# Kernel optimization log

Hardware: AMD Instinct MI355X
Metric: run time of the kernel (lower is better)

## Reference

```python
import jax, jax.numpy as jnp
import numpy as np

F_DIM = 256; H = 4; LAT = 256; BOT = 128
B = 64; NPG = 180; N = B * NPG; E = N * 16; HF = H * F_DIM
NEG_SLOPE = 0.2  # PyG GATConv default LeakyReLU slope


def _gat(x, src, dst, W, att_s, att_d, bias):
    # PyG GATConv (concat=True): h = x W, per-edge score LeakyReLU(a_s[src]+a_d[dst]),
    # softmax over incoming edges of each dst, weighted sum, concat heads, + bias.
    h = (x @ W).reshape(N, H, F_DIM)
    a_s = jnp.einsum('nhc,hc->nh', h, att_s)
    a_d = jnp.einsum('nhc,hc->nh', h, att_d)
    e = jax.nn.leaky_relu(a_s[src] + a_d[dst], NEG_SLOPE)          # [E+N, H]
    m = jax.ops.segment_max(e, dst, num_segments=N)                # stable softmax per dst
    p = jnp.exp(e - m[dst])
    s = jax.ops.segment_sum(p, dst, num_segments=N)
    alpha = p / (s[dst] + 1e-16)
    out = jax.ops.segment_sum(alpha[:, :, None] * h[src], dst, num_segments=N)
    return out.reshape(N, HF) + bias


def setup_inputs() -> dict:
    key = jax.random.key(0)
    ks = jax.random.split(key, 40)
    def rn(i, shape, scale):
        return jax.random.normal(ks[i], shape, jnp.float32) * jnp.float32(scale)
    inp = {}
    inp['z'] = jax.random.normal(ks[0], (B, LAT), jnp.float32)
    inp['condition'] = jax.random.normal(ks[1], (B, BOT), jnp.float32)
    dst = jax.random.randint(ks[2], (E,), 0, N)
    off = jax.random.randint(ks[3], (E,), 1, NPG)
    src = (dst + off) % N  # no self-loops by construction (PyG adds them itself)
    inp['edge_index'] = jnp.stack([src, dst]).astype(jnp.int32)
    inp['batch'] = jnp.repeat(jnp.arange(B, dtype=jnp.int32), NPG)
    def lin(i, fin, fout):
        s = 1.0 / np.sqrt(fin)
        return rn(i, (fin, fout), s), rn(i + 1, (fout,), s)
    inp['W_init'], inp['b_init'] = lin(4, LAT + BOT, F_DIM)
    inp['W1'] = rn(6, (F_DIM + 180, HF), 1.0 / np.sqrt(F_DIM + 180))
    inp['as1'] = rn(7, (H, F_DIM), 0.1); inp['ad1'] = rn(8, (H, F_DIM), 0.1)
    inp['b1'] = rn(9, (HF,), 0.1)
    inp['W2'] = rn(10, (HF, HF), 1.0 / np.sqrt(HF))
    inp['as2'] = rn(11, (H, F_DIM), 0.1); inp['ad2'] = rn(12, (H, F_DIM), 0.1)
    inp['b2'] = rn(13, (HF,), 0.1)
    inp['W3'] = rn(14, (HF, HF), 1.0 / np.sqrt(HF))
    inp['as3'] = rn(15, (H, F_DIM), 0.1); inp['ad3'] = rn(16, (H, F_DIM), 0.1)
    inp['b3'] = rn(17, (HF,), 0.1)
    inp['Wp'], inp['bp'] = lin(18, HF, F_DIM)
    inp['Wfp'], inp['bfp'] = lin(20, F_DIM, 2)
    inp['Ws'], inp['bs'] = lin(22, HF, F_DIM)
    inp['Wfs'], inp['bfs'] = lin(24, F_DIM, 2)
    inp['Wt'], inp['bt'] = lin(26, HF, F_DIM)
    inp['Wft'], inp['bft'] = lin(28, F_DIM, 1)
    return inp


def reference(z, condition, edge_index, batch, W_init, b_init,
              W1, as1, ad1, b1, W2, as2, ad2, b2, W3, as3, ad3, b3,
              Wp, bp, Wfp, bfp, Ws, bs, Wfs, bfs, Wt, bt, Wft, bft):
    zc = jnp.concatenate([z, condition], axis=1) @ W_init + b_init  # [B, F]
    x = zc[batch]                                                    # [N, F]
    # node order within each (sorted) batch segment -> one-hot(180)
    start = jnp.searchsorted(batch, jnp.arange(B, dtype=batch.dtype))
    order = jnp.arange(N) - start[batch]
    pos = jax.nn.one_hot(order, 180, dtype=x.dtype)
    x = jax.nn.relu(jnp.concatenate([x, pos], axis=1))               # [N, F+180]
    # add self loops (PyG GATConv default add_self_loops=True)
    loops = jnp.arange(N, dtype=edge_index.dtype)
    src = jnp.concatenate([edge_index[0], loops])
    dst = jnp.concatenate([edge_index[1], loops])
    x = jax.nn.relu(_gat(x, src, dst, W1, as1, ad1, b1))
    x = jax.nn.relu(_gat(x, src, dst, W2, as2, ad2, b2))
    x = jax.nn.relu(_gat(x, src, dst, W3, as3, ad3, b3))
    out_pos = jax.nn.relu(x @ Wp + bp) @ Wfp + bfp     # [N, 2]
    out_size = jax.nn.relu(x @ Ws + bs) @ Wfs + bfs    # [N, 2]
    out_theta = jax.nn.relu(x @ Wt + bt) @ Wft + bft   # [N, 1]
    return out_pos, out_size, out_theta
```

## Files before the change

### kernel.cpp

```cpp
#include <hip/hip_runtime.h>
#include <hip/hip_bf16.h>

#define NODES 11520
#define EDGES 184320
#define NB    64
#define NPG   180
#define CAP   64

typedef __bf16 bf16x8 __attribute__((ext_vector_type(8)));
typedef __bf16 bf16x4 __attribute__((ext_vector_type(4)));
typedef float  f32x4  __attribute__((ext_vector_type(4)));

__global__ __launch_bounds__(256) void k_init(
    const float* __restrict__ z, const float* __restrict__ cond,
    const float* __restrict__ Wi, const float* __restrict__ bi,
    const float* __restrict__ W1, float* __restrict__ Y1)
{
    __shared__ float xr[384];
    __shared__ float part[4][256];
    __shared__ float zr[256];
    const int b = blockIdx.x, t = threadIdx.x;
    xr[t] = (t < 256) ? z[b * 256 + t] : 0.f;
    if (t < 128) xr[256 + t] = cond[b * 128 + t];
    __syncthreads();
    {
        const int kq = t >> 6, tc = t & 63;
        f32x4 acc = {0.f, 0.f, 0.f, 0.f};
        const float* wbase = Wi + (size_t)(kq * 96) * 256 + 4 * tc;
        const float* xb = xr + kq * 96;
#pragma unroll 8
        for (int k = 0; k < 96; ++k) {
            const float4 w = *(const float4*)(wbase + (size_t)k * 256);
            const float x = xb[k];
            acc[0] = fmaf(x, w.x, acc[0]);
            acc[1] = fmaf(x, w.y, acc[1]);
            acc[2] = fmaf(x, w.z, acc[2]);
            acc[3] = fmaf(x, w.w, acc[3]);
        }
        *(f32x4*)&part[kq][4 * tc] = acc;
    }
    __syncthreads();
    zr[t] = fmaxf(bi[t] + part[0][t] + part[1][t] + part[2][t] + part[3][t], 0.f);
    __syncthreads();
    {
        f32x4 acc = {0.f, 0.f, 0.f, 0.f};
#pragma unroll 8
        for (int k = 0; k < 256; ++k) {
            const float4 w = *(const float4*)(W1 + (size_t)k * 1024 + 4 * t);
            const float x = zr[k];
            acc[0] = fmaf(x, w.x, acc[0]);
            acc[1] = fmaf(x, w.y, acc[1]);
            acc[2] = fmaf(x, w.z, acc[2]);
            acc[3] = fmaf(x, w.w, acc[3]);
        }
        *(f32x4*)(Y1 + (size_t)b * 1024 + 4 * t) = acc;
    }
}

__global__ __launch_bounds__(256) void k_h1(
    const float* __restrict__ Y1, const float* __restrict__ W1,
    const float* __restrict__ atts, const float* __restrict__ attd,
    __bf16* __restrict__ hb, float* __restrict__ asb, float* __restrict__ adb,
    float* __restrict__ zas, float* __restrict__ zad)
{
    const int n = blockIdx.x, t = threadIdx.x;
    if (t < 4)      zas[n * 4 + t] = 0.f;
    else if (t < 8) zad[n * 4 + (t - 4)] = 0.f;
    const int g = n / NPG, o = n - g * NPG;
    const float4 y = *(const float4*)(Y1 + (size_t)g * 1024 + 4 * t);
    const float4 w = *(const float4*)(W1 + (size_t)(256 + o) * 1024 + 4 * t);
    const float4 h = {y.x + w.x, y.y + w.y, y.z + w.z, y.w + w.w};
    bf16x4 hv = {(__bf16)h.x, (__bf16)h.y, (__bf16)h.z, (__bf16)h.w};
    *(bf16x4*)(hb + (size_t)n * 1024 + 4 * t) = hv;
    const int head = t >> 6, c0 = (t & 63) * 4;
    const float4 s4 = *(const float4*)(atts + head * 256 + c0);
    const float4 d4 = *(const float4*)(attd + head * 256 + c0);
    float ps = h.x * s4.x + h.y * s4.y + h.z * s4.z + h.w * s4.w;
    float pd = h.x * d4.x + h.y * d4.y + h.z * d4.z + h.w * d4.w;
    for (int off = 32; off; off >>= 1) {
        ps += __shfl_xor(ps, off, 64);
        pd += __shfl_xor(pd, off, 64);
    }
    if ((t & 63) == 0) { asb[n * 4 + head] = ps; adb[n * 4 + head] = pd; }
}

__global__ __launch_bounds__(256) void k_hist(
    const int* __restrict__ ei, int* __restrict__ counts,
    int* __restrict__ bucket)
{
    const int e = blockIdx.x * 256 + threadIdx.x;
    if (e >= EDGES) return;
    const int s = ei[e], d = ei[EDGES + e];
    const int pos = atomicAdd(&counts[d], 1);
    if (pos < CAP) bucket[(size_t)d * CAP + pos] = s;
}

__global__ __launch_bounds__(256) void k_agg(
    const __bf16* __restrict__ hb, const float* __restrict__ asb,
    const float* __restrict__ adb, const int* __restrict__ counts,
    const int* __restrict__ bucket, const float* __restrict__ bias,
    __bf16* __restrict__ xout, float* __restrict__ zas, float* __restrict__ zad)
{
    const int b = blockIdx.x;
    const int nb = (b & 7) * (NODES / 8) + 2 * (b >> 3);
    const int t = threadIdx.x;
    const int half = t >> 7, tt = t & 127;
    const int n = nb + half;
    __shared__ float sc[2][CAP + 1][4];
    __shared__ int   ssrc[2][CAP + 1];
    __shared__ float sinv[2][4];
    if (zas != nullptr) {
        if (t < 8)       zas[nb * 4 + t] = 0.f;
        else if (t < 16) zad[nb * 4 + (t - 8)] = 0.f;
    }
    const int deg = min(counts[n], CAP);
    const int ne  = deg + 1;
    if (tt < deg)       ssrc[half][tt] = bucket[(size_t)n * CAP + tt];
    else if (tt == deg) ssrc[half][tt] = n;
    __syncthreads();
    if (tt < ne) {
        const int s = ssrc[half][tt];
        const float4 as4 = *(const float4*)(asb + (size_t)s * 4);
        const float4 ad4 = *(const float4*)(adb + (size_t)n * 4);
        const float v0 = as4.x + ad4.x, v1 = as4.y + ad4.y;
        const float v2 = as4.z + ad4.z, v3 = as4.w + ad4.w;
        sc[half][tt][0] = v0 > 0.f ? v0 : 0.2f * v0;
        sc[half][tt][1] = v1 > 0.f ? v1 : 0.2f * v1;
        sc[half][tt][2] = v2 > 0.f ? v2 : 0.2f * v2;
        sc[half][tt][3] = v3 > 0.f ? v3 : 0.2f * v3;
    }
    __syncthreads();
    const int ln = t & 63, hw = (t >> 6) & 1;
#pragma unroll
    for (int hh = 0; hh < 2; ++hh) {
        const int head = hw * 2 + hh;
        float m = -1e30f;
        for (int k = ln; k < ne; k += 64) m = fmaxf(m, sc[half][k][head]);
        for (int off = 32; off; off >>= 1) m = fmaxf(m, __shfl_xor(m, off, 64));
        float s = 0.f;
        for (int k = ln; k < ne; k += 64) {
            const float p = __expf(sc[half][k][head] - m);
            sc[half][k][head] = p;
            s += p;
        }
        for (int off = 32; off; off >>= 1) s += __shfl_xor(s, off, 64);
        if (ln == 0) sinv[half][head] = 1.f / (s + 1e-16f);
    }
    __syncthreads();
    const int j0 = tt * 8, hd = tt >> 5;
    const float inv = sinv[half][hd];
    float a[8] = {0, 0, 0, 0, 0, 0, 0, 0};
    int k = 0;
    for (; k + 4 <= ne; k += 4) {
        float al[4]; bf16x8 hv[4];
#pragma unroll
        for (int u = 0; u < 4; ++u) {
            al[u] = sc[half][k + u][hd] * inv;
            hv[u] = *(const bf16x8*)(hb + (size_t)ssrc[half][k + u] * 1024 + j0);
        }
#pragma unroll
        for (int u = 0; u < 4; ++u)
#pragma unroll
            for (int e = 0; e < 8; ++e)
                a[e] = fmaf(al[u], (float)hv[u][e], a[e]);
    }
    for (; k < ne; ++k) {
        const float al = sc[half][k][hd] * inv;
        const bf16x8 hv = *(const bf16x8*)(hb + (size_t)ssrc[half][k] * 1024 + j0);
#pragma unroll
        for (int e = 0; e < 8; ++e)
            a[e] = fmaf(al, (float)hv[e], a[e]);
    }
    const float4 b4a = *(const float4*)(bias + j0);
    const float4 b4b = *(const float4*)(bias + j0 + 4);
    bf16x8 o;
    o[0] = (__bf16)fmaxf(a[0] + b4a.x, 0.f);
    o[1] = (__bf16)fmaxf(a[1] + b4a.y, 0.f);
    o[2] = (__bf16)fmaxf(a[2] + b4a.z, 0.f);
    o[3] = (__bf16)fmaxf(a[3] + b4a.w, 0.f);
    o[4] = (__bf16)fmaxf(a[4] + b4b.x, 0.f);
    o[5] = (__bf16)fmaxf(a[5] + b4b.y, 0.f);
    o[6] = (__bf16)fmaxf(a[6] + b4b.z, 0.f);
    o[7] = (__bf16)fmaxf(a[7] + b4b.w, 0.f);
    *(bf16x8*)(xout + (size_t)n * 1024 + j0) = o;
}

__global__ __launch_bounds__(256) void k_transW(
    const float* __restrict__ W2, const float* __restrict__ W3,
    __bf16* __restrict__ W2t, __bf16* __restrict__ W3t)
{
    const float* W = blockIdx.z ? W3 : W2;
    __bf16* WT = blockIdx.z ? W3t : W2t;
    __shared__ float t[32][33];
    const int n0 = blockIdx.x * 32, k0 = blockIdx.y * 32;
    const int tx = threadIdx.x & 31, ty = threadIdx.x >> 5;
#pragma unroll
    for (int i = 0; i < 32; i += 8)
        t[ty + i][tx] = W[(size_t)(k0 + ty + i) * 1024 + n0 + tx];
    __syncthreads();
#pragma unroll
    for (int i = 0; i < 32; i += 8)
        WT[(size_t)(n0 + ty + i) * 1024 + k0 + tx] = (__bf16)t[tx][ty + i];
}

__global__ __launch_bounds__(256) void k_transH(
    const float* __restrict__ Wp, const float* __restrict__ Ws,
    const float* __restrict__ Wt, __bf16* __restrict__ WHt,
    const float* __restrict__ bp, const float* __restrict__ bs,
    const float* __restrict__ bt, float* __restrict__ bc)
{
    if (blockIdx.x == 8) {
        if (blockIdx.y == 0) {
            const int t = blockIdx.z * 256 + threadIdx.x;
            const float v = blockIdx.z == 0 ? bp[threadIdx.x]
                          : blockIdx.z == 1 ? bs[threadIdx.x] : bt[threadIdx.x];
            bc[t] = v;
        }
        return;
    }
    const float* W = blockIdx.z == 0 ? Wp : blockIdx.z == 1 ? Ws : Wt;
    __bf16* WT = WHt + (size_t)blockIdx.z * 256 * 1024;
    __shared__ float t[32][33];
    const int n0 = blockIdx.x * 32, k0 = blockIdx.y * 32;
    const int tx = threadIdx.x & 31, ty = threadIdx.x >> 5;
#pragma unroll
    for (int i = 0; i < 32; i += 8)
        t[ty + i][tx] = W[(size_t)(k0 + ty + i) * 256 + n0 + tx];
    __syncthreads();
#pragma unroll
    for (int i = 0; i < 32; i += 8)
        WT[(size_t)(n0 + ty + i) * 1024 + k0 + tx] = (__bf16)t[tx][ty + i];
}

#define STAGE(kbase)                                                           \
    {                                                                          \
        _Pragma("unroll")                                                      \
        for (int h = 0; h < 2; ++h) {                                          \
            _Pragma("unroll")                                                  \
            for (int cc = 0; cc < 2; ++cc) {                                   \
                const int c = 2 * w + cc;                                      \
                const int row = c * 16 + lr;                                   \
                __builtin_amdgcn_global_load_lds(                              \
                    (const __attribute__((address_space(1))) void*)            \
                        (A + (size_t)(m0 + row) * K + (kbase) + h * 32 + lk),  \
                    (__attribute__((address_space(3))) void*)                  \
                        (As + h * 4096 + c * 512), 16, 0, 0);                  \
                __builtin_amdgcn_global_load_lds(                              \
                    (const __attribute__((address_space(1))) void*)            \
                        (BT + (size_t)(n0 + row) * K + (kbase) + h * 32 + lk), \
                    (__attribute__((address_space(3))) void*)                  \
                        (Bs + h * 4096 + c * 512), 16, 0, 0);                  \
            }                                                                  \
        }                                                                      \
    }

#define GEMM_MAINLOOP()                                                        \
    f32x4 acc[4][4];                                                           \
    _Pragma("unroll")                                                          \
    for (int i = 0; i < 4; ++i)                                                \
        _Pragma("unroll")                                                      \
        for (int j = 0; j < 4; ++j)                                            \
            acc[i][j] = (f32x4){0.f, 0.f, 0.f, 0.f};                           \
    for (int k0 = 0; k0 < K; k0 += 64) {                                       \
        STAGE(k0);                                                             \
        __syncthreads();                                                       \
        _Pragma("unroll")                                                      \
        for (int h = 0; h < 2; ++h) {                                          \
            bf16x8 af[4], bfr[4];                                              \
            _Pragma("unroll")                                                  \
            for (int i = 0; i < 4; ++i)                                        \
                af[i] = *(const bf16x8*)(As + h * 4096 +                       \
                                         (wm + i * 16 + r16) * 32 + quad * 8); \
            _Pragma("unroll")                                                  \
            for (int j = 0; j < 4; ++j)                                        \
                bfr[j] = *(const bf16x8*)(Bs + h * 4096 +                      \
                                          (wn + j * 16 + r16) * 32 + quad * 8);\
            _Pragma("unroll")                                                  \
            for (int i = 0; i < 4; ++i)                                        \
                _Pragma("unroll")                                              \
                for (int j = 0; j < 4; ++j)                                    \
                    acc[i][j] = __builtin_amdgcn_mfma_f32_16x16x32_bf16(       \
                        af[i], bfr[j], acc[i][j], 0, 0, 0);                    \
        }                                                                      \
        __syncthreads();                                                       \
    }

__global__ __launch_bounds__(256) void gemm_bf16_h(
    const __bf16* __restrict__ A, const __bf16* __restrict__ BT,
    __bf16* __restrict__ Cb,
    const float* __restrict__ atts, const float* __restrict__ attd,
    float* __restrict__ asb, float* __restrict__ adb,
    int M, int N, int K)
{
    const int lb = blockIdx.x;
    const int g = lb & 7, idx = lb >> 3;
    const int bx = idx & 7;
    const int by = (idx >> 3) * 8 + g;
    if (by * 128 >= M) return;
    const int m0 = by * 128, n0 = bx * 128;

    __shared__ __bf16 As[2 * 128 * 32];
    __shared__ __bf16 Bs[2 * 128 * 32];
    const int tid = threadIdx.x;
    const int w = tid >> 6, l = tid & 63;
    const int lr = l >> 2, lk = (l & 3) * 8;
    const int quad = l >> 4, r16 = l & 15;
    const int wm = (w >> 1) * 64, wn = (w & 1) * 64;

    GEMM_MAINLOOP();

    const int head = (n0 + wn) >> 8;
    float sa[4], da[4];
#pragma unroll
    for (int j = 0; j < 4; ++j) {
        const int cl = (n0 + wn + j * 16 + r16) & 255;
        sa[j] = atts[head * 256 + cl];
        da[j] = attd[head * 256 + cl];
    }
#pragma unroll
    for (int i = 0; i < 4; ++i) {
#pragma unroll
        for (int r = 0; r < 4; ++r) {
            const int mg = m0 + wm + i * 16 + quad * 4 + r;
            float ps = 0.f, pd = 0.f;
#pragma unroll
            for (int j = 0; j < 4; ++j) {
                const int ng = n0 + wn + j * 16 + r16;
                const float v = acc[i][j][r];
                ps = fmaf(v, sa[j], ps);
                pd = fmaf(v, da[j], pd);
                Cb[(size_t)mg * N + ng] = (__bf16)v;
            }
            for (int off = 8; off; off >>= 1) {
                ps += __shfl_xor(ps, off, 64);
                pd += __shfl_xor(pd, off, 64);
            }
            if (r16 == 0) {
                atomicAdd(&asb[mg * 4 + head], ps);
                atomicAdd(&adb[mg * 4 + head], pd);
            }
        }
    }
}

__global__ __launch_bounds__(256) void gemm_heads(
    const __bf16* __restrict__ A, const __bf16* __restrict__ BT,
    const float* __restrict__ biascat,
    const float* __restrict__ Wfp, const float* __restrict__ bfp,
    const float* __restrict__ Wfs, const float* __restrict__ bfs,
    const float* __restrict__ Wft, const float* __restrict__ bft,
    float* __restrict__ out, int M, int K)
{
    const int lb = blockIdx.x;
    const int g = lb & 7, idx = lb >> 3;
    const int bx = idx % 6;
    const int by = (idx / 6) * 8 + g;
    if (by * 128 >= M) return;
    const int m0 = by * 128, n0 = bx * 128;

    __shared__ __bf16 As[2 * 128 * 32];
    __shared__ __bf16 Bs[2 * 128 * 32];
    const int tid = threadIdx.x;
    const int w = tid >> 6, l = tid & 63;
    const int lr = l >> 2, lk = (l & 3) * 8;
    const int quad = l >> 4, r16 = l & 15;
    const int wm = (w >> 1) * 64, wn = (w & 1) * 64;

    GEMM_MAINLOOP();

    const int hg = bx >> 1;
    const float* Wf = hg == 0 ? Wfp : hg == 1 ? Wfs : Wft;
    const int nout = hg == 2 ? 1 : 2;
    float wf0[4], wf1[4], bz[4];
#pragma unroll
    for (int j = 0; j < 4; ++j) {
        const int ng = n0 + wn + j * 16 + r16;
        const int cl = ng & 255;
        bz[j]  = biascat[ng];
        wf0[j] = Wf[cl * nout];
        wf1[j] = nout == 2 ? Wf[cl * nout + 1] : 0.f;
    }
    const bool addb = ((bx & 1) == 0) && (wn == 0);
    const float fb0 = hg == 0 ? bfp[0] : hg == 1 ? bfs[0] : bft[0];
    const float fb1 = hg == 2 ? 0.f : (hg == 0 ? bfp[1] : bfs[1]);
#pragma unroll
    for (int i = 0; i < 4; ++i) {
#pragma unroll
        for (int r = 0; r < 4; ++r) {
            const int mg = m0 + wm + i * 16 + quad * 4 + r;
            float o0 = 0.f, o1 = 0.f;
#pragma unroll
            for (int j = 0; j < 4; ++j) {
                const float v = fmaxf(acc[i][j][r] + bz[j], 0.f);
                o0 = fmaf(v, wf0[j], o0);
                o1 = fmaf(v, wf1[j], o1);
            }
            for (int off = 8; off; off >>= 1) {
                o0 += __shfl_xor(o0, off, 64);
                o1 += __shfl_xor(o1, off, 64);
            }
            if (r16 == 0) {
                if (addb) { o0 += fb0; o1 += fb1; }
                const size_t base = hg == 0 ? 2 * (size_t)mg
                                 : hg == 1 ? 2 * (size_t)NODES + 2 * (size_t)mg
                                 : 4 * (size_t)NODES + (size_t)mg;
                atomicAdd(&out[base], o0);
                if (nout == 2) atomicAdd(&out[base + 1], o1);
            }
        }
    }
}

extern "C" void kernel_launch(void* const* d_in, const int* in_sizes, int n_in,
                              void* d_out, int out_size, void* d_ws, size_t ws_size,
                              hipStream_t stream)
{
    const float* z    = (const float*)d_in[0];
    const float* cond = (const float*)d_in[1];
    const int*   ei   = (const int*)  d_in[2];
    const float* Wi   = (const float*)d_in[4];
    const float* bi   = (const float*)d_in[5];
    const float* W1   = (const float*)d_in[6];
    const float* as1  = (const float*)d_in[7];
    const float* ad1  = (const float*)d_in[8];
    const float* b1   = (const float*)d_in[9];
    const float* W2   = (const float*)d_in[10];
    const float* as2  = (const float*)d_in[11];
    const float* ad2  = (const float*)d_in[12];
    const float* b2   = (const float*)d_in[13];
    const float* W3   = (const float*)d_in[14];
    const float* as3  = (const float*)d_in[15];
    const float* ad3  = (const float*)d_in[16];
    const float* b3   = (const float*)d_in[17];
    const float* Wp   = (const float*)d_in[18];
    const float* bp   = (const float*)d_in[19];
    const float* Wfp  = (const float*)d_in[20];
    const float* bfp  = (const float*)d_in[21];
    const float* Ws   = (const float*)d_in[22];
    const float* bs   = (const float*)d_in[23];
    const float* Wfs  = (const float*)d_in[24];
    const float* bfs  = (const float*)d_in[25];
    const float* Wt   = (const float*)d_in[26];
    const float* bt   = (const float*)d_in[27];
    const float* Wft  = (const float*)d_in[28];
    const float* bft  = (const float*)d_in[29];
    float* out = (float*)d_out;

    char* p = (char*)d_ws;
    __bf16* hb    = (__bf16*)p;           p += (size_t)NODES * 1024 * 2;
    __bf16* xb16  = (__bf16*)p;           p += (size_t)NODES * 1024 * 2;
    float* asA    = (float*)p;            p += (size_t)NODES * 4 * 4;
    float* adA    = (float*)p;            p += (size_t)NODES * 4 * 4;
    float* asB    = (float*)p;            p += (size_t)NODES * 4 * 4;
    float* adB    = (float*)p;            p += (size_t)NODES * 4 * 4;
    float* Y1     = (float*)p;            p += 64 * 1024 * 4;
    int*   counts = (int*)p;              p += (size_t)NODES * 4;
    int*   bucket = (int*)p;              p += (size_t)NODES * CAP * 4;
    __bf16* W2t   = (__bf16*)p;           p += (size_t)1024 * 1024 * 2;
    __bf16* W3t   = (__bf16*)p;           p += (size_t)1024 * 1024 * 2;
    __bf16* WHt   = (__bf16*)p;           p += (size_t)768 * 1024 * 2;
    float* biascat= (float*)p;            p += 768 * 4;

    hipMemsetAsync(out, 0, (size_t)out_size * sizeof(float), stream);
    hipMemsetAsync(counts, 0, NODES * sizeof(int), stream);

    k_transW<<<dim3(32, 32, 2), 256, 0, stream>>>(W2, W3, W2t, W3t);
    k_transH<<<dim3(9, 32, 3), 256, 0, stream>>>(Wp, Ws, Wt, WHt,
                                                 bp, bs, bt, biascat);
    k_hist<<<EDGES / 256, 256, 0, stream>>>(ei, counts, bucket);

    k_init<<<NB, 256, 0, stream>>>(z, cond, Wi, bi, W1, Y1);
    k_h1<<<NODES, 256, 0, stream>>>(Y1, W1, as1, ad1, hb, asA, adA, asB, adB);
    k_agg<<<NODES / 2, 256, 0, stream>>>(hb, asA, adA, counts, bucket, b1,
                                         xb16, nullptr, nullptr);

    gemm_bf16_h<<<8 * 96, 256, 0, stream>>>(xb16, W2t, hb, as2, ad2,
                                            asB, adB, NODES, 1024, 1024);
    k_agg<<<NODES / 2, 256, 0, stream>>>(hb, asB, adB, counts, bucket, b2,
                                         xb16, asA, adA);
    gemm_bf16_h<<<8 * 96, 256, 0, stream>>>(xb16, W3t, hb, as3, ad3,
                                            asA, adA, NODES, 1024, 1024);
    k_agg<<<NODES / 2, 256, 0, stream>>>(hb, asA, adA, counts, bucket, b3,
                                         xb16, nullptr, nullptr);

    gemm_heads<<<6 * 96, 256, 0, stream>>>(xb16, WHt, biascat,
                                           Wfp, bfp, Wfs, bfs, Wft, bft,
                                           out, NODES, 1024);
}
```

Baseline: 377.8 us.

## Merge prep kernels into one launch and deepen aggregation gather unroll

Folds the weight transposes, head-weight transpose with bias concat, edge bucketing, and initial MLP into a single block-indexed k_prep kernel. This removes three kernel launches and lets the independent prep work run concurrently on the device. The k_agg gather loop now unrolls 8 neighbor loads instead of 4 to put more memory requests in flight, at the cost of more registers and a longer remainder loop.

```diff
diff --git a/kernel.cpp b/kernel.cpp
--- a/kernel.cpp
+++ b/kernel.cpp
@@ -11,49 +11,109 @@
 typedef __bf16 bf16x4 __attribute__((ext_vector_type(4)));
 typedef float  f32x4  __attribute__((ext_vector_type(4)));
 
-__global__ __launch_bounds__(256) void k_init(
+__global__ __launch_bounds__(256) void k_prep(
+    const float* __restrict__ W2, const float* __restrict__ W3,
+    __bf16* __restrict__ W2t, __bf16* __restrict__ W3t,
+    const float* __restrict__ Wp, const float* __restrict__ Ws,
+    const float* __restrict__ Wt, __bf16* __restrict__ WHt,
+    const float* __restrict__ bp, const float* __restrict__ bs,
+    const float* __restrict__ bt, float* __restrict__ bc,
+    const int* __restrict__ ei, int* __restrict__ counts,
+    int* __restrict__ bucket,
     const float* __restrict__ z, const float* __restrict__ cond,
     const float* __restrict__ Wi, const float* __restrict__ bi,
     const float* __restrict__ W1, float* __restrict__ Y1)
 {
-    __shared__ float xr[384];
-    __shared__ float part[4][256];
-    __shared__ float zr[256];
+    __shared__ union {
+        float tr[32][33];
+        struct { float xr[384]; float part[4][256]; float zr[256]; } init;
+    } sm;
     const int b = blockIdx.x, t = threadIdx.x;
-    xr[t] = (t < 256) ? z[b * 256 + t] : 0.f;
-    if (t < 128) xr[256 + t] = cond[b * 128 + t];
-    __syncthreads();
+
+    if (b < 2048) {
+        const float* W = (b >= 1024) ? W3 : W2;
+        __bf16* WT = (b >= 1024) ? W3t : W2t;
+        const int rem = b & 1023;
+        const int n0 = (rem & 31) * 32, k0 = (rem >> 5) * 32;
+        const int tx = t & 31, ty = t >> 5;
+#pragma unroll
+        for (int i = 0; i < 32; i += 8)
+            sm.tr[ty + i][tx] = W[(size_t)(k0 + ty + i) * 1024 + n0 + tx];
+        __syncthreads();
+#pragma unroll
+        for (int i = 0; i < 32; i += 8)
+            WT[(size_t)(n0 + ty + i) * 1024 + k0 + tx] = (__bf16)sm.tr[tx][ty + i];
+        return;
+    }
+    if (b < 2912) {
+        const int idx = b - 2048;
+        const int zz = idx / 288, r2 = idx % 288;
+        const int x = r2 % 9, y = r2 / 9;
+        if (x == 8) {
+            if (y == 0) {
+                const float v = zz == 0 ? bp[t] : zz == 1 ? bs[t] : bt[t];
+                bc[zz * 256 + t] = v;
+            }
+            return;
+        }
+        const float* W = zz == 0 ? Wp : zz == 1 ? Ws : Wt;
+        __bf16* WT = WHt + (size_t)zz * 256 * 1024;
+        const int n0 = x * 32, k0 = y * 32;
+        const int tx = t & 31, ty = t >> 5;
+#pragma unroll
+        for (int i = 0; i < 32; i += 8)
+            sm.tr[ty + i][tx] = W[(size_t)(k0 + ty + i) * 256 + n0 + tx];
+        __syncthreads();
+#pragma unroll
+        for (int i = 0; i < 32; i += 8)
+            WT[(size_t)(n0 + ty + i) * 1024 + k0 + tx] = (__bf16)sm.tr[tx][ty + i];
+        return;
+    }
+    if (b < 3632) {
+        const int e = (b - 2912) * 256 + t;
+        const int s = ei[e], d = ei[EDGES + e];
+        const int pos = atomicAdd(&counts[d], 1);
+        if (pos < CAP) bucket[(size_t)d * CAP + pos] = s;
+        return;
+    }
     {
-        const int kq = t >> 6, tc = t & 63;
-        f32x4 acc = {0.f, 0.f, 0.f, 0.f};
-        const float* wbase = Wi + (size_t)(kq * 96) * 256 + 4 * tc;
-        const float* xb = xr + kq * 96;
+        const int bb = b - 3632;
+        sm.init.xr[t] = (t < 256) ? z[bb * 256 + t] : 0.f;
+        if (t < 128) sm.init.xr[256 + t] = cond[bb * 128 + t];
+        __syncthreads();
+        {
+            const int kq = t >> 6, tc = t & 63;
+            f32x4 acc = {0.f, 0.f, 0.f, 0.f};
+            const float* wbase = Wi + (size_t)(kq * 96) * 256 + 4 * tc;
+            const float* xb = sm.init.xr + kq * 96;
 #pragma unroll 8
-        for (int k = 0; k < 96; ++k) {
-            const float4 w = *(const float4*)(wbase + (size_t)k * 256);
-            const float x = xb[k];
-            acc[0] = fmaf(x, w.x, acc[0]);
-            acc[1] = fmaf(x, w.y, acc[1]);
-            acc[2] = fmaf(x, w.z, acc[2]);
-            acc[3] = fmaf(x, w.w, acc[3]);
-        }
-        *(f32x4*)&part[kq][4 * tc] = acc;
-    }
-    __syncthreads();
-    zr[t] = fmaxf(bi[t] + part[0][t] + part[1][t] + part[2][t] + part[3][t], 0.f);
-    __syncthreads();
-    {
-        f32x4 acc = {0.f, 0.f, 0.f, 0.f};
+            for (int k = 0; k < 96; ++k) {
+                const float4 w = *(const float4*)(wbase + (size_t)k * 256);
+                const float x = xb[k];
+                acc[0] = fmaf(x, w.x, acc[0]);
+                acc[1] = fmaf(x, w.y, acc[1]);
+                acc[2] = fmaf(x, w.z, acc[2]);
+                acc[3] = fmaf(x, w.w, acc[3]);
+            }
+            *(f32x4*)&sm.init.part[kq][4 * tc] = acc;
+        }
+        __syncthreads();
+        sm.init.zr[t] = fmaxf(bi[t] + sm.init.part[0][t] + sm.init.part[1][t] +
+                              sm.init.part[2][t] + sm.init.part[3][t], 0.f);
+        __syncthreads();
+        {
+            f32x4 acc = {0.f, 0.f, 0.f, 0.f};
 #pragma unroll 8
-        for (int k = 0; k < 256; ++k) {
-            const float4 w = *(const float4*)(W1 + (size_t)k * 1024 + 4 * t);
-            const float x = zr[k];
-            acc[0] = fmaf(x, w.x, acc[0]);
-            acc[1] = fmaf(x, w.y, acc[1]);
-            acc[2] = fmaf(x, w.z, acc[2]);
-            acc[3] = fmaf(x, w.w, acc[3]);
-        }
-        *(f32x4*)(Y1 + (size_t)b * 1024 + 4 * t) = acc;
+            for (int k = 0; k < 256; ++k) {
+                const float4 w = *(const float4*)(W1 + (size_t)k * 1024 + 4 * t);
+                const float x = sm.init.zr[k];
+                acc[0] = fmaf(x, w.x, acc[0]);
+                acc[1] = fmaf(x, w.y, acc[1]);
+                acc[2] = fmaf(x, w.z, acc[2]);
+                acc[3] = fmaf(x, w.w, acc[3]);
+            }
+            *(f32x4*)(Y1 + (size_t)bb * 1024 + 4 * t) = acc;
+        }
     }
 }
 
@@ -84,17 +144,6 @@
     if ((t & 63) == 0) { asb[n * 4 + head] = ps; adb[n * 4 + head] = pd; }
 }
 
-__global__ __launch_bounds__(256) void k_hist(
-    const int* __restrict__ ei, int* __restrict__ counts,
-    int* __restrict__ bucket)
-{
-    const int e = blockIdx.x * 256 + threadIdx.x;
-    if (e >= EDGES) return;
-    const int s = ei[e], d = ei[EDGES + e];
-    const int pos = atomicAdd(&counts[d], 1);
-    if (pos < CAP) bucket[(size_t)d * CAP + pos] = s;
-}
-
 __global__ __launch_bounds__(256) void k_agg(
     const __bf16* __restrict__ hb, const float* __restrict__ asb,
     const float* __restrict__ adb, const int* __restrict__ counts,
@@ -151,15 +200,15 @@
     const float inv = sinv[half][hd];
     float a[8] = {0, 0, 0, 0, 0, 0, 0, 0};
     int k = 0;
-    for (; k + 4 <= ne; k += 4) {
-        float al[4]; bf16x8 hv[4];
-#pragma unroll
-        for (int u = 0; u < 4; ++u) {
+    for (; k + 8 <= ne; k += 8) {
+        float al[8]; bf16x8 hv[8];
+#pragma unroll
+        for (int u = 0; u < 8; ++u) {
             al[u] = sc[half][k + u][hd] * inv;
             hv[u] = *(const bf16x8*)(hb + (size_t)ssrc[half][k + u] * 1024 + j0);
         }
 #pragma unroll
-        for (int u = 0; u < 4; ++u)
+        for (int u = 0; u < 8; ++u)
 #pragma unroll
             for (int e = 0; e < 8; ++e)
                 a[e] = fmaf(al[u], (float)hv[u][e], a[e]);
@@ -183,53 +232,6 @@
     o[6] = (__bf16)fmaxf(a[6] + b4b.z, 0.f);
     o[7] = (__bf16)fmaxf(a[7] + b4b.w, 0.f);
     *(bf16x8*)(xout + (size_t)n * 1024 + j0) = o;
-}
-
-__global__ __launch_bounds__(256) void k_transW(
-    const float* __restrict__ W2, const float* __restrict__ W3,
-    __bf16* __restrict__ W2t, __bf16* __restrict__ W3t)
-{
-    const float* W = blockIdx.z ? W3 : W2;
-    __bf16* WT = blockIdx.z ? W3t : W2t;
-    __shared__ float t[32][33];
-    const int n0 = blockIdx.x * 32, k0 = blockIdx.y * 32;
-    const int tx = threadIdx.x & 31, ty = threadIdx.x >> 5;
-#pragma unroll
-    for (int i = 0; i < 32; i += 8)
-        t[ty + i][tx] = W[(size_t)(k0 + ty + i) * 1024 + n0 + tx];
-    __syncthreads();
-#pragma unroll
-    for (int i = 0; i < 32; i += 8)
-        WT[(size_t)(n0 + ty + i) * 1024 + k0 + tx] = (__bf16)t[tx][ty + i];
-}
-
-__global__ __launch_bounds__(256) void k_transH(
-    const float* __restrict__ Wp, const float* __restrict__ Ws,
-    const float* __restrict__ Wt, __bf16* __restrict__ WHt,
-    const float* __restrict__ bp, const float* __restrict__ bs,
-    const float* __restrict__ bt, float* __restrict__ bc)
-{
-    if (blockIdx.x == 8) {
-        if (blockIdx.y == 0) {
-            const int t = blockIdx.z * 256 + threadIdx.x;
-            const float v = blockIdx.z == 0 ? bp[threadIdx.x]
-                          : blockIdx.z == 1 ? bs[threadIdx.x] : bt[threadIdx.x];
-            bc[t] = v;
-        }
-        return;
-    }
-    const float* W = blockIdx.z == 0 ? Wp : blockIdx.z == 1 ? Ws : Wt;
-    __bf16* WT = WHt + (size_t)blockIdx.z * 256 * 1024;
-    __shared__ float t[32][33];
-    const int n0 = blockIdx.x * 32, k0 = blockIdx.y * 32;
-    const int tx = threadIdx.x & 31, ty = threadIdx.x >> 5;
-#pragma unroll
-    for (int i = 0; i < 32; i += 8)
-        t[ty + i][tx] = W[(size_t)(k0 + ty + i) * 256 + n0 + tx];
-    __syncthreads();
-#pragma unroll
-    for (int i = 0; i < 32; i += 8)
-        WT[(size_t)(n0 + ty + i) * 1024 + k0 + tx] = (__bf16)t[tx][ty + i];
 }
 
 #define STAGE(kbase)                                                           \
@@ -464,12 +466,11 @@
     hipMemsetAsync(out, 0, (size_t)out_size * sizeof(float), stream);
     hipMemsetAsync(counts, 0, NODES * sizeof(int), stream);
 
-    k_transW<<<dim3(32, 32, 2), 256, 0, stream>>>(W2, W3, W2t, W3t);
-    k_transH<<<dim3(9, 32, 3), 256, 0, stream>>>(Wp, Ws, Wt, WHt,
-                                                 bp, bs, bt, biascat);
-    k_hist<<<EDGES / 256, 256, 0, stream>>>(ei, counts, bucket);
-
-    k_init<<<NB, 256, 0, stream>>>(z, cond, Wi, bi, W1, Y1);
+    k_prep<<<3696, 256, 0, stream>>>(W2, W3, W2t, W3t,
+                                     Wp, Ws, Wt, WHt, bp, bs, bt, biascat,
+                                     ei, counts, bucket,
+                                     z, cond, Wi, bi, W1, Y1);
+
     k_h1<<<NODES, 256, 0, stream>>>(Y1, W1, as1, ad1, hb, asA, adA, asB, adB);
     k_agg<<<NODES / 2, 256, 0, stream>>>(hb, asA, adA, counts, bucket, b1,
                                          xb16, nullptr, nullptr);
```

Result: slower. 385.6 us (+2.1%).
